# Performance work log

Hardware: AMD Instinct MI355X
Metric: run time of the kernel (lower is better)

Reference implementation:

```python
import jax, jax.numpy as jnp
import numpy as np
import math

B, S, D, H = 4, 1024, 4096, 32
HD = D // H  # 128


def _rope(t, cos, sin):
    # t: [B,S,H,HD]; cos/sin: [S, HD//2]
    tr = t.reshape(*t.shape[:-1], HD // 2, 2)
    re, im = tr[..., 0], tr[..., 1]
    c = cos[None, :, None, :]
    s = sin[None, :, None, :]
    out_re = re * c - im * s
    out_im = re * s + im * c
    return jnp.stack([out_re, out_im], axis=-1).reshape(t.shape)


def setup_inputs() -> dict:
    key = jax.random.key(0)
    ks = jax.random.split(key, 6)
    wscale = 1.0 / math.sqrt(D)
    x = jax.random.normal(ks[0], (B, S, D), dtype=jnp.float32)
    wq = jax.random.normal(ks[1], (D, D), dtype=jnp.float32) * wscale
    wk = jax.random.normal(ks[2], (D, D), dtype=jnp.float32) * wscale
    wv = jax.random.normal(ks[3], (D, D), dtype=jnp.float32) * wscale
    wo = jax.random.normal(ks[4], (D, D), dtype=jnp.float32) * wscale
    # standard LLaMA RoPE frequencies: theta = 10000^{-2i/HD}
    inv_freq = 1.0 / (10000.0 ** (np.arange(0, HD, 2, dtype=np.float32) / HD))
    angles = np.arange(S, dtype=np.float32)[:, None] * inv_freq[None, :]  # [S, HD//2]
    freqs_cos = jnp.asarray(np.cos(angles), dtype=jnp.float32)
    freqs_sin = jnp.asarray(np.sin(angles), dtype=jnp.float32)
    # causal mask, additive, 0 on/below diagonal, -inf above
    mask = jnp.where(jnp.tril(jnp.ones((S, S), dtype=bool)), 0.0, -jnp.inf)
    mask = mask[None, None].astype(jnp.float32)  # [1,1,S,S]
    return {"x": x, "wq": wq, "wk": wk, "wv": wv, "wo": wo,
            "freqs_cos": freqs_cos, "freqs_sin": freqs_sin, "mask": mask}


def reference(x, wq, wk, wv, wo, freqs_cos, freqs_sin, mask):
    # projections (torch Linear: y = x @ W^T)
    xq = (x @ wq.T).reshape(B, S, H, HD)
    xk = (x @ wk.T).reshape(B, S, H, HD)
    xv = (x @ wv.T).reshape(B, S, H, HD)
    xq = _rope(xq, freqs_cos, freqs_sin)
    xk = _rope(xk, freqs_cos, freqs_sin)
    # prefill (start_pos == 0): keys/values are xk/xv
    scores = jnp.einsum('bshd,bthd->bhst', xq, xk) / math.sqrt(HD)
    scores = scores + mask
    probs = jax.nn.softmax(scores.astype(jnp.float32), axis=-1).astype(xq.dtype)
    out = jnp.einsum('bhst,bthd->bshd', probs, xv).reshape(B, S, D)
    return out @ wo.T
```

## Files before the change

### kernel.cpp

```cpp
#include <hip/hip_runtime.h>
#include <hip/hip_bf16.h>


typedef __bf16 bf16_t;
typedef bf16_t bf16x8 __attribute__((ext_vector_type(8)));
typedef bf16_t bf16x4 __attribute__((ext_vector_type(4)));
typedef bf16_t bf16x2 __attribute__((ext_vector_type(2)));
typedef float  f32x4  __attribute__((ext_vector_type(4)));

#define DDIM 4096
#define NEG_INF (-__builtin_inff())

__device__ __forceinline__ void gl_lds16(const bf16_t* g, bf16_t* l) {
    __builtin_amdgcn_global_load_lds((__attribute__((address_space(1))) void*)(g),
                                     (__attribute__((address_space(3))) void*)(l), 16, 0, 0);
}

__global__ __launch_bounds__(256)
void cvt_k(const float* __restrict__ src, bf16_t* __restrict__ dst, int n8)
{
    const int stride = gridDim.x * 256;
    for (int i = blockIdx.x * 256 + threadIdx.x; i < n8; i += stride) {
        const float* s = src + (size_t)i * 8;
        f32x4 a = *(const f32x4*)(s);
        f32x4 b = *(const f32x4*)(s + 4);
        bf16x8 o;
        o[0] = (bf16_t)a.x; o[1] = (bf16_t)a.y; o[2] = (bf16_t)a.z; o[3] = (bf16_t)a.w;
        o[4] = (bf16_t)b.x; o[5] = (bf16_t)b.y; o[6] = (bf16_t)b.z; o[7] = (bf16_t)b.w;
        *(bf16x8*)(dst + (size_t)i * 8) = o;
    }
}

template<bool C_F32>
__global__ __launch_bounds__(256, 2)
void gemm_bb(const bf16_t* __restrict__ A, const bf16_t* __restrict__ Bm, void* __restrict__ Cv)
{
    constexpr int BK = 64;
    __shared__ __attribute__((aligned(16))) bf16_t sA[128 * BK];
    __shared__ __attribute__((aligned(16))) bf16_t sB[128 * BK];

    const int tid  = threadIdx.x;
    const int wave = tid >> 6, lane = tid & 63;
    const int quad = lane >> 4, r = lane & 15;
    const int wm = (wave >> 1) << 6, wn = (wave & 1) << 6;
    const int m0 = blockIdx.y << 7, n0 = blockIdx.x << 7;

    const int scol = (lane & 7) << 3;
    const bf16_t* gA = A  + (size_t)(m0 + wave * 32 + (lane >> 3)) * DDIM + scol;
    const bf16_t* gB = Bm + (size_t)(n0 + wave * 32 + (lane >> 3)) * DDIM + scol;
    bf16_t* lA = sA + wave * 2048;
    bf16_t* lB = sB + wave * 2048;

    f32x4 acc[4][4] = {};

    for (int kt = 0; kt < DDIM; kt += BK) {
#pragma unroll
        for (int i = 0; i < 4; ++i) {
            gl_lds16(gA + (size_t)(i * 8) * DDIM + kt, lA + i * 512);
            gl_lds16(gB + (size_t)(i * 8) * DDIM + kt, lB + i * 512);
        }
        __syncthreads();
#pragma unroll
        for (int kk = 0; kk < BK; kk += 32) {
            bf16x8 af[4], bfr[4];
#pragma unroll
            for (int i = 0; i < 4; ++i)
                af[i] = *(const bf16x8*)(sA + (wm + i * 16 + r) * BK + kk + quad * 8);
#pragma unroll
            for (int j = 0; j < 4; ++j)
                bfr[j] = *(const bf16x8*)(sB + (wn + j * 16 + r) * BK + kk + quad * 8);
#pragma unroll
            for (int i = 0; i < 4; ++i)
#pragma unroll
                for (int j = 0; j < 4; ++j)
                    acc[i][j] = __builtin_amdgcn_mfma_f32_16x16x32_bf16(af[i], bfr[j], acc[i][j], 0, 0, 0);
        }
        __syncthreads();
    }
#pragma unroll
    for (int i = 0; i < 4; ++i) {
#pragma unroll
        for (int reg = 0; reg < 4; ++reg) {
            const size_t row = (size_t)(m0 + wm + i * 16 + quad * 4 + reg) * DDIM;
#pragma unroll
            for (int j = 0; j < 4; ++j) {
                const size_t idx = row + n0 + wn + j * 16 + r;
                if constexpr (C_F32) ((float*)Cv)[idx] = acc[i][j][reg];
                else                 ((bf16_t*)Cv)[idx] = (bf16_t)acc[i][j][reg];
            }
        }
    }
}

__global__ void rope_k(bf16_t* __restrict__ q, bf16_t* __restrict__ k,
                       const float* __restrict__ fc, const float* __restrict__ fs)
{
    const int p   = blockIdx.x * 256 + threadIdx.x;
    const int bs  = p >> 11;
    const int rem = p & 2047;
    const int s   = bs & 1023;
    const int h   = rem >> 6;
    const int pp  = rem & 63;
    const size_t off = (size_t)bs * DDIM + h * 128 + pp * 2;
    const float c  = fc[s * 64 + pp];
    const float sn = fs[s * 64 + pp];
    bf16x2 qv = *(bf16x2*)(q + off);
    bf16x2 kv = *(bf16x2*)(k + off);
    const float qre = (float)qv.x, qim = (float)qv.y;
    const float kre = (float)kv.x, kim = (float)kv.y;
    bf16x2 qo, ko;
    qo.x = (bf16_t)(qre * c - qim * sn);
    qo.y = (bf16_t)(qre * sn + qim * c);
    ko.x = (bf16_t)(kre * c - kim * sn);
    ko.y = (bf16_t)(kre * sn + kim * c);
    *(bf16x2*)(q + off) = qo;
    *(bf16x2*)(k + off) = ko;
}

__global__ __launch_bounds__(256, 2)
void attn_k(const bf16_t* __restrict__ qm, const bf16_t* __restrict__ km,
            const bf16_t* __restrict__ vm, bf16_t* __restrict__ om)
{
    constexpr int BQ = 128, BT = 64;
    constexpr int PS = 80;
    __shared__ __attribute__((aligned(16))) bf16_t sK[BT * 128];
    __shared__ __attribute__((aligned(16))) bf16_t sVt[128 * 64];
    __shared__ __attribute__((aligned(16))) bf16_t sP[4][32 * PS];
    const int tid = threadIdx.x, wave = tid >> 6, lane = tid & 63;
    const int quad = lane >> 4, r = lane & 15;
    const int b = blockIdx.x >> 5, h = blockIdx.x & 31;
    const int q0 = (7 - (int)blockIdx.y) * BQ;
    const int qw = q0 + wave * 32;
    const float scale = 0.08838834764831845f;

    bf16x8 qf[2][4];
#pragma unroll
    for (int mt = 0; mt < 2; ++mt)
#pragma unroll
        for (int kk = 0; kk < 4; ++kk)
            qf[mt][kk] = *(const bf16x8*)(qm + (size_t)(b * 1024 + qw + mt * 16 + r) * DDIM
                                          + h * 128 + kk * 32 + quad * 8);

    f32x4 oacc[2][8] = {};
    float m_i[2][4], l_i[2][4];
#pragma unroll
    for (int mt = 0; mt < 2; ++mt)
#pragma unroll
        for (int reg = 0; reg < 4; ++reg) { m_i[mt][reg] = NEG_INF; l_i[mt][reg] = 0.f; }

    const bf16_t* gKb = km + (size_t)(b * 1024 + wave * 16 + quad) * DDIM + h * 128;
    const int rp = tid >> 3, cseg = tid & 7;

    for (int t0 = 0; t0 < q0 + BQ; t0 += BT) {
#pragma unroll
        for (int i = 0; i < 4; ++i) {
            const int xv = (i * 4 + quad) & 7;
            gl_lds16(gKb + (size_t)(t0 + i * 4) * DDIM + ((r ^ xv) << 3),
                     sK + (wave * 4 + i) * 512);
        }
        {
            const bf16_t* gv = vm + (size_t)(b * 1024 + t0 + 2 * rp) * DDIM + h * 128 + cseg * 16;
            bf16x8 v00 = *(const bf16x8*)(gv);
            bf16x8 v01 = *(const bf16x8*)(gv + 8);
            bf16x8 v10 = *(const bf16x8*)(gv + DDIM);
            bf16x8 v11 = *(const bf16x8*)(gv + DDIM + 8);
#pragma unroll
            for (int e = 0; e < 8; ++e) {
                bf16x2 w0, w1;
                w0.x = v00[e]; w0.y = v10[e];
                w1.x = v01[e]; w1.y = v11[e];
                const int pb = ((((rp >> 2) ^ (e ^ cseg)) & 7) << 3) + ((rp & 3) << 1);
                *(bf16x2*)(sVt + (cseg * 16 + e) * 64 + pb) = w0;
                *(bf16x2*)(sVt + (cseg * 16 + 8 + e) * 64 + pb) = w1;
            }
        }
        __syncthreads();

        f32x4 sacc[2][4] = {};
#pragma unroll
        for (int kk = 0; kk < 4; ++kk) {
            bf16x8 kf[4];
#pragma unroll
            for (int nt = 0; nt < 4; ++nt)
                kf[nt] = *(const bf16x8*)(sK + (nt * 16 + r) * 128
                                          + (((kk * 4 + quad) ^ (r & 7)) << 3));
#pragma unroll
            for (int mt = 0; mt < 2; ++mt)
#pragma unroll
                for (int nt = 0; nt < 4; ++nt)
                    sacc[mt][nt] = __builtin_amdgcn_mfma_f32_16x16x32_bf16(qf[mt][kk], kf[nt], sacc[mt][nt], 0, 0, 0);
        }

#pragma unroll
        for (int mt = 0; mt < 2; ++mt) {
#pragma unroll
            for (int reg = 0; reg < 4; ++reg) {
                const int qrow = qw + mt * 16 + quad * 4 + reg;
                float mx = NEG_INF;
#pragma unroll
                for (int nt = 0; nt < 4; ++nt) {
                    const int tcol = t0 + nt * 16 + r;
                    float v = sacc[mt][nt][reg] * scale;
                    v = (tcol <= qrow) ? v : NEG_INF;
                    sacc[mt][nt][reg] = v;
                    mx = fmaxf(mx, v);
                }
                mx = fmaxf(mx, __shfl_xor(mx, 1));
                mx = fmaxf(mx, __shfl_xor(mx, 2));
                mx = fmaxf(mx, __shfl_xor(mx, 4));
                mx = fmaxf(mx, __shfl_xor(mx, 8));
                if (!__all(mx - m_i[mt][reg] <= 8.0f)) {
                    const float mnew = fmaxf(m_i[mt][reg], mx);
                    const float alpha = __expf(m_i[mt][reg] - mnew);
                    m_i[mt][reg] = mnew;
                    l_i[mt][reg] *= alpha;
#pragma unroll
                    for (int nt = 0; nt < 8; ++nt)
                        oacc[mt][nt][reg] *= alpha;
                }
                float rs = 0.f;
#pragma unroll
                for (int nt = 0; nt < 4; ++nt) {
                    const float pv = __expf(sacc[mt][nt][reg] - m_i[mt][reg]);
                    rs += pv;
                    sP[wave][(mt * 16 + quad * 4 + reg) * PS + nt * 16 + r] = (bf16_t)pv;
                }
                rs += __shfl_xor(rs, 1);
                rs += __shfl_xor(rs, 2);
                rs += __shfl_xor(rs, 4);
                rs += __shfl_xor(rs, 8);
                l_i[mt][reg] += rs;
            }
        }

#pragma unroll
        for (int kk2 = 0; kk2 < 2; ++kk2) {
            bf16x8 pf[2];
#pragma unroll
            for (int mt = 0; mt < 2; ++mt)
                pf[mt] = *(const bf16x8*)(&sP[wave][(mt * 16 + r) * PS + kk2 * 32 + quad * 8]);
#pragma unroll
            for (int nt = 0; nt < 8; ++nt) {
                bf16x8 vf = *(const bf16x8*)(sVt + (nt * 16 + r) * 64
                                             + ((((kk2 * 4 + quad) ^ (r & 7) ^ nt) & 7) << 3));
#pragma unroll
                for (int mt = 0; mt < 2; ++mt)
                    oacc[mt][nt] = __builtin_amdgcn_mfma_f32_16x16x32_bf16(pf[mt], vf, oacc[mt][nt], 0, 0, 0);
            }
        }
        __syncthreads();
    }

#pragma unroll
    for (int mt = 0; mt < 2; ++mt)
#pragma unroll
        for (int reg = 0; reg < 4; ++reg) {
            const float inv = 1.0f / l_i[mt][reg];
            const size_t row = (size_t)(b * 1024 + qw + mt * 16 + quad * 4 + reg) * DDIM + h * 128;
#pragma unroll
            for (int nt = 0; nt < 8; ++nt)
                om[row + nt * 16 + r] = (bf16_t)(oacc[mt][nt][reg] * inv);
        }
}

extern "C" void kernel_launch(void* const* d_in, const int* in_sizes, int n_in,
                              void* d_out, int out_size, void* d_ws, size_t ws_size,
                              hipStream_t stream)
{
    (void)in_sizes; (void)n_in; (void)out_size; (void)d_ws; (void)ws_size;
    const float* x  = (const float*)d_in[0];
    const float* wq = (const float*)d_in[1];
    const float* wk = (const float*)d_in[2];
    const float* wv = (const float*)d_in[3];
    const float* wo = (const float*)d_in[4];
    const float* fc = (const float*)d_in[5];
    const float* fs = (const float*)d_in[6];

    const size_t NE = (size_t)DDIM * DDIM;
    const int n8 = (int)(NE / 8);

    bf16_t* wkb = (bf16_t*)d_out;
    bf16_t* wvb = wkb + NE;
    bf16_t* xb  = (bf16_t*)d_in[2];
    bf16_t* wqb = xb + NE;
    bf16_t* wob = (bf16_t*)d_in[3];
    bf16_t* ob  = wob + NE;
    bf16_t* kb  = (bf16_t*)d_in[1];
    bf16_t* vb  = kb + NE;
    bf16_t* qb  = (bf16_t*)d_in[4];
    float*  out = (float*)d_out;

    cvt_k<<<2048, 256, 0, stream>>>(wk, wkb, n8);
    cvt_k<<<2048, 256, 0, stream>>>(wv, wvb, n8);
    cvt_k<<<2048, 256, 0, stream>>>(x,  xb,  n8);
    cvt_k<<<2048, 256, 0, stream>>>(wq, wqb, n8);
    cvt_k<<<2048, 256, 0, stream>>>(wo, wob, n8);

    const dim3 gg(32, 32, 1);
    gemm_bb<false><<<gg, 256, 0, stream>>>(xb, wkb, kb);
    gemm_bb<false><<<gg, 256, 0, stream>>>(xb, wvb, vb);
    gemm_bb<false><<<gg, 256, 0, stream>>>(xb, wqb, qb);
    rope_k<<<32768, 256, 0, stream>>>(qb, kb, fc, fs);
    attn_k<<<dim3(128, 8), 256, 0, stream>>>(qb, kb, vb, ob);
    gemm_bb<true><<<gg, 256, 0, stream>>>(ob, wob, out);
}
```

Before: 1.021 ms.

## Replace GEMM with 256x256-tile, 8-wave, double-buffered pipelined MFMA kernel

```diff
diff --git a/kernel.cpp b/kernel.cpp
--- a/kernel.cpp
+++ b/kernel.cpp
@@ -9,7 +9,9 @@
 typedef float  f32x4  __attribute__((ext_vector_type(4)));
 
 #define DDIM 4096
+#define NTILES 64
 #define NEG_INF (-__builtin_inff())
+#define MFMA16(a,b,c) __builtin_amdgcn_mfma_f32_16x16x32_bf16(a,b,c,0,0,0)
 
 __device__ __forceinline__ void gl_lds16(const bf16_t* g, bf16_t* l) {
     __builtin_amdgcn_global_load_lds((__attribute__((address_space(1))) void*)(g),
@@ -31,65 +33,145 @@
     }
 }
 
+
+__device__ __forceinline__ void stage_half(const bf16_t* __restrict__ A,
+    const bf16_t* __restrict__ Bm, int m0, int n0, int kt, int hh,
+    bf16_t* __restrict__ sb, int wave, int lane)
+{
+#pragma unroll
+    for (int j = 0; j < 2; ++j) {
+        const int chunk = wave * 2 + j;
+        int row0;
+        if (hh == 0)      row0 = chunk * 8;
+        else if (hh == 1) row0 = 128 + chunk * 8;
+        else if (hh == 2) row0 = (chunk < 8) ? chunk * 8 : 64 + chunk * 8;
+        else              row0 = (chunk < 8) ? 64 + chunk * 8 : 128 + chunk * 8;
+        const bool isB = (hh < 2);
+        const int grow = (isB ? n0 : m0) + row0 + (lane >> 3);
+        const int gcol = kt + (((lane & 7) ^ (lane >> 3)) << 3);
+        const bf16_t* gp = (isB ? Bm : A) + (size_t)grow * DDIM + gcol;
+        gl_lds16(gp, sb + (isB ? 16384 : 0) + row0 * 64);
+    }
+}
+
+template<int STG>
+__device__ __forceinline__ void ktile(const bf16_t* __restrict__ A,
+    const bf16_t* __restrict__ Bm, int m0, int n0, int t,
+    bf16_t* __restrict__ sb, bf16_t* __restrict__ sbn,
+    int wave, int lane, int quad, int r, int wm, int wn,
+    f32x4 acc[4][2][4], bf16x8 bfrag[4][2])
+{
+    const int kx0 = (quad ^ (r & 7)) << 3;
+    const int kx1 = ((4 + quad) ^ (r & 7)) << 3;
+    {
+        bf16x8 af[2][2];
+#pragma unroll
+        for (int nf = 0; nf < 4; ++nf) {
+            const int ro = 16384 + (((wn << 6) + (nf << 4) + r) << 6);
+            bfrag[nf][0] = *(const bf16x8*)(sb + ro + kx0);
+            bfrag[nf][1] = *(const bf16x8*)(sb + ro + kx1);
+        }
+#pragma unroll
+        for (int mf = 0; mf < 2; ++mf) {
+            const int ro = ((wm << 7) + (mf << 4) + r) << 6;
+            af[mf][0] = *(const bf16x8*)(sb + ro + kx0);
+            af[mf][1] = *(const bf16x8*)(sb + ro + kx1);
+        }
+        if (STG >= 1) stage_half(A, Bm, m0, n0, (t + 1) << 6, 3, sbn, wave, lane);
+        __builtin_amdgcn_sched_barrier(0);
+        __builtin_amdgcn_s_barrier();
+        asm volatile("s_waitcnt lgkmcnt(0)" ::: "memory");
+        __builtin_amdgcn_sched_barrier(0);
+        __builtin_amdgcn_s_setprio(1);
+#pragma unroll
+        for (int kk = 0; kk < 2; ++kk)
+#pragma unroll
+            for (int mf = 0; mf < 2; ++mf)
+#pragma unroll
+                for (int nf = 0; nf < 4; ++nf)
+                    acc[0][mf][nf] = MFMA16(af[mf][kk], bfrag[nf][kk], acc[0][mf][nf]);
+        __builtin_amdgcn_s_setprio(0);
+        __builtin_amdgcn_sched_barrier(0);
+        __builtin_amdgcn_s_barrier();
+    }
+#pragma unroll
+    for (int q = 1; q < 4; ++q) {
+        bf16x8 af[2][2];
+#pragma unroll
+        for (int mf = 0; mf < 2; ++mf) {
+            const int ro = ((wm << 7) + (q << 5) + (mf << 4) + r) << 6;
+            af[mf][0] = *(const bf16x8*)(sb + ro + kx0);
+            af[mf][1] = *(const bf16x8*)(sb + ro + kx1);
+        }
+        if (STG == 2) stage_half(A, Bm, m0, n0, (t + 2) << 6, q - 1, sb, wave, lane);
+        __builtin_amdgcn_sched_barrier(0);
+        __builtin_amdgcn_s_barrier();
+        asm volatile("s_waitcnt lgkmcnt(0)" ::: "memory");
+        __builtin_amdgcn_sched_barrier(0);
+        __builtin_amdgcn_s_setprio(1);
+#pragma unroll
+        for (int kk = 0; kk < 2; ++kk)
+#pragma unroll
+            for (int mf = 0; mf < 2; ++mf)
+#pragma unroll
+                for (int nf = 0; nf < 4; ++nf)
+                    acc[q][mf][nf] = MFMA16(af[mf][kk], bfrag[nf][kk], acc[q][mf][nf]);
+        __builtin_amdgcn_s_setprio(0);
+        if (q == 3) {
+            if (STG == 2)      asm volatile("s_waitcnt vmcnt(6)" ::: "memory");
+            else if (STG == 1) asm volatile("s_waitcnt vmcnt(0)" ::: "memory");
+        }
+        __builtin_amdgcn_sched_barrier(0);
+        __builtin_amdgcn_s_barrier();
+    }
+}
+
 template<bool C_F32>
-__global__ __launch_bounds__(256, 2)
-void gemm_bb(const bf16_t* __restrict__ A, const bf16_t* __restrict__ Bm, void* __restrict__ Cv)
-{
-    constexpr int BK = 64;
-    __shared__ __attribute__((aligned(16))) bf16_t sA[128 * BK];
-    __shared__ __attribute__((aligned(16))) bf16_t sB[128 * BK];
-
+__global__ __launch_bounds__(512, 2)
+void gemm256(const bf16_t* __restrict__ A, const bf16_t* __restrict__ Bm, void* __restrict__ Cv)
+{
+    __shared__ __attribute__((aligned(16))) bf16_t sm[2 * 32768];
     const int tid  = threadIdx.x;
     const int wave = tid >> 6, lane = tid & 63;
     const int quad = lane >> 4, r = lane & 15;
-    const int wm = (wave >> 1) << 6, wn = (wave & 1) << 6;
-    const int m0 = blockIdx.y << 7, n0 = blockIdx.x << 7;
-
-    const int scol = (lane & 7) << 3;
-    const bf16_t* gA = A  + (size_t)(m0 + wave * 32 + (lane >> 3)) * DDIM + scol;
-    const bf16_t* gB = Bm + (size_t)(n0 + wave * 32 + (lane >> 3)) * DDIM + scol;
-    bf16_t* lA = sA + wave * 2048;
-    bf16_t* lB = sB + wave * 2048;
-
-    f32x4 acc[4][4] = {};
-
-    for (int kt = 0; kt < DDIM; kt += BK) {
-#pragma unroll
-        for (int i = 0; i < 4; ++i) {
-            gl_lds16(gA + (size_t)(i * 8) * DDIM + kt, lA + i * 512);
-            gl_lds16(gB + (size_t)(i * 8) * DDIM + kt, lB + i * 512);
-        }
-        __syncthreads();
-#pragma unroll
-        for (int kk = 0; kk < BK; kk += 32) {
-            bf16x8 af[4], bfr[4];
-#pragma unroll
-            for (int i = 0; i < 4; ++i)
-                af[i] = *(const bf16x8*)(sA + (wm + i * 16 + r) * BK + kk + quad * 8);
-#pragma unroll
-            for (int j = 0; j < 4; ++j)
-                bfr[j] = *(const bf16x8*)(sB + (wn + j * 16 + r) * BK + kk + quad * 8);
-#pragma unroll
-            for (int i = 0; i < 4; ++i)
-#pragma unroll
-                for (int j = 0; j < 4; ++j)
-                    acc[i][j] = __builtin_amdgcn_mfma_f32_16x16x32_bf16(af[i], bfr[j], acc[i][j], 0, 0, 0);
-        }
-        __syncthreads();
-    }
-#pragma unroll
-    for (int i = 0; i < 4; ++i) {
-#pragma unroll
-        for (int reg = 0; reg < 4; ++reg) {
-            const size_t row = (size_t)(m0 + wm + i * 16 + quad * 4 + reg) * DDIM;
-#pragma unroll
-            for (int j = 0; j < 4; ++j) {
-                const size_t idx = row + n0 + wn + j * 16 + r;
-                if constexpr (C_F32) ((float*)Cv)[idx] = acc[i][j][reg];
-                else                 ((bf16_t*)Cv)[idx] = (bf16_t)acc[i][j][reg];
+    const int wm = wave >> 2, wn = wave & 3;
+    const int swz = ((int)blockIdx.x % 8) * 32 + (int)blockIdx.x / 8;
+    const int m0 = (swz >> 4) << 8, n0 = (swz & 15) << 8;
+
+    f32x4 acc[4][2][4] = {};
+    bf16x8 bfrag[4][2];
+
+#pragma unroll
+    for (int hh = 0; hh < 4; ++hh) stage_half(A, Bm, m0, n0, 0, hh, sm, wave, lane);
+#pragma unroll
+    for (int hh = 0; hh < 3; ++hh) stage_half(A, Bm, m0, n0, 64, hh, sm + 32768, wave, lane);
+    asm volatile("s_waitcnt vmcnt(6)" ::: "memory");
+    __builtin_amdgcn_s_barrier();
+
+#pragma unroll 2
+    for (int t = 0; t < NTILES - 2; ++t) {
+        bf16_t* sb  = sm + ((t & 1) ? 32768 : 0);
+        bf16_t* sbn = sm + ((t & 1) ? 0 : 32768);
+        ktile<2>(A, Bm, m0, n0, t, sb, sbn, wave, lane, quad, r, wm, wn, acc, bfrag);
+    }
+    ktile<1>(A, Bm, m0, n0, NTILES - 2, sm, sm + 32768, wave, lane, quad, r, wm, wn, acc, bfrag);
+    ktile<0>(A, Bm, m0, n0, NTILES - 1, sm + 32768, sm, wave, lane, quad, r, wm, wn, acc, bfrag);
+
+#pragma unroll
+    for (int q = 0; q < 4; ++q)
+#pragma unroll
+        for (int mf = 0; mf < 2; ++mf)
+#pragma unroll
+            for (int reg = 0; reg < 4; ++reg) {
+                const size_t row = (size_t)(m0 + (wm << 7) + (q << 5) + (mf << 4)
+                                            + (quad << 2) + reg) * DDIM;
+#pragma unroll
+                for (int nf = 0; nf < 4; ++nf) {
+                    const size_t idx = row + n0 + (wn << 6) + (nf << 4) + r;
+                    if constexpr (C_F32) ((float*)Cv)[idx] = acc[q][mf][nf][reg];
+                    else                 ((bf16_t*)Cv)[idx] = (bf16_t)acc[q][mf][nf][reg];
+                }
             }
-        }
-    }
 }
 
 __global__ void rope_k(bf16_t* __restrict__ q, bf16_t* __restrict__ k,
@@ -188,7 +270,7 @@
             for (int mt = 0; mt < 2; ++mt)
 #pragma unroll
                 for (int nt = 0; nt < 4; ++nt)
-                    sacc[mt][nt] = __builtin_amdgcn_mfma_f32_16x16x32_bf16(qf[mt][kk], kf[nt], sacc[mt][nt], 0, 0, 0);
+                    sacc[mt][nt] = MFMA16(qf[mt][kk], kf[nt], sacc[mt][nt]);
         }
 
 #pragma unroll
@@ -245,7 +327,7 @@
                                              + ((((kk2 * 4 + quad) ^ (r & 7) ^ nt) & 7) << 3));
 #pragma unroll
                 for (int mt = 0; mt < 2; ++mt)
-                    oacc[mt][nt] = __builtin_amdgcn_mfma_f32_16x16x32_bf16(pf[mt], vf, oacc[mt][nt], 0, 0, 0);
+                    oacc[mt][nt] = MFMA16(pf[mt], vf, oacc[mt][nt]);
             }
         }
         __syncthreads();
@@ -296,11 +378,10 @@
     cvt_k<<<2048, 256, 0, stream>>>(wq, wqb, n8);
     cvt_k<<<2048, 256, 0, stream>>>(wo, wob, n8);
 
-    const dim3 gg(32, 32, 1);
-    gemm_bb<false><<<gg, 256, 0, stream>>>(xb, wkb, kb);
-    gemm_bb<false><<<gg, 256, 0, stream>>>(xb, wvb, vb);
-    gemm_bb<false><<<gg, 256, 0, stream>>>(xb, wqb, qb);
+    gemm256<false><<<256, 512, 0, stream>>>(xb, wkb, kb);
+    gemm256<false><<<256, 512, 0, stream>>>(xb, wvb, vb);
+    gemm256<false><<<256, 512, 0, stream>>>(xb, wqb, qb);
     rope_k<<<32768, 256, 0, stream>>>(qb, kb, fc, fs);
     attn_k<<<dim3(128, 8), 256, 0, stream>>>(qb, kb, vb, ob);
-    gemm_bb<true><<<gg, 256, 0, stream>>>(ob, wob, out);
-}
+    gemm256<true><<<256, 512, 0, stream>>>(ob, wob, out);
+}
```

Result: faster. 851.9 us (-16.6%).
